# Kernel optimization log

Measured on AMD Instinct MI355X. Metric: run time of the kernel, lower is better.

Reference implementation:

```python
import jax, jax.numpy as jnp
import numpy as np

IN_DIM = 1024
OUT_DIM = 1024
NUM_COEFFS = 32 + 3  # grid_size + spline_order


def setup_inputs() -> dict:
    key = jax.random.key(0)
    k1, k2, k3 = jax.random.split(key, 3)
    x = jax.random.normal(k1, (4096, IN_DIM), dtype=jnp.float32)
    spline_weight = jax.random.normal(k2, (IN_DIM, OUT_DIM, NUM_COEFFS), dtype=jnp.float32) * 0.1
    base_scale = jax.random.normal(k3, (IN_DIM, OUT_DIM), dtype=jnp.float32) * 0.1
    grid = jnp.linspace(-1.0, 1.0, NUM_COEFFS, dtype=jnp.float32)
    return {"x": x, "spline_weight": spline_weight, "base_scale": base_scale, "grid": grid}


def _b_spline_cubic(x, grid):
    # x: [b, i] -> basis [b, i, c]
    h = 2.0 / (NUM_COEFFS - 1)
    dist = jnp.abs(x[..., None] - grid) / h
    inner = 2.0 / 3.0 - dist * dist + dist * dist * dist * 0.5
    t = 2.0 - dist
    outer = t * t * t / 6.0
    return jnp.where(dist < 1.0, inner, jnp.where(dist < 2.0, outer, 0.0))


def reference(x, spline_weight, base_scale, grid):
    x_norm = jnp.clip(x, -0.99, 0.99)
    base_act = jax.nn.silu(x_norm)                      # [b, i]
    base_out = jnp.einsum('bi,ij->bj', base_act, base_scale)
    basis = _b_spline_cubic(x_norm, grid)               # [b, i, c]
    spline_out = jnp.einsum('bic,ijc->bj', basis, spline_weight)
    return base_out + spline_out
```

## Files before the change

### kernel.cpp

```cpp
#include <hip/hip_runtime.h>
#include <hip/hip_bf16.h>


#define IN_DIM 1024
#define OUT_DIM 1024
#define NC 35
#define KPI 36
#define KTOT (IN_DIM * KPI)
#define NW (KTOT / 32)
#define MROWS 4096
#define BM 256
#define BN 256
#define BK 32
#define NSPLIT 4
#define WPC (NW / NSPLIT)

typedef __attribute__((ext_vector_type(8))) __bf16 bf16x8;
typedef __attribute__((ext_vector_type(4))) float f32x4;

__device__ __forceinline__ unsigned short f2bf(float f) {
  unsigned int u = __builtin_bit_cast(unsigned int, f);
  u = (u + 0x7FFFu + ((u >> 16) & 1u)) >> 16;
  return (unsigned short)u;
}

__device__ __forceinline__ uint4 pack8(const unsigned short* v) {
  uint4 t4;
  t4.x = (unsigned)v[0] | ((unsigned)v[1] << 16);
  t4.y = (unsigned)v[2] | ((unsigned)v[3] << 16);
  t4.z = (unsigned)v[4] | ((unsigned)v[5] << 16);
  t4.w = (unsigned)v[6] | ((unsigned)v[7] << 16);
  return t4;
}

__global__ __launch_bounds__(256) void prep_w2(const float* __restrict__ sw,
                                               const float* __restrict__ bs,
                                               unsigned short* __restrict__ w2) {
  const int tid = threadIdx.x;
  const int w = blockIdx.x;
  const int n = blockIdx.y * 256 + tid;
  const int k0 = w * 32;
  const int i0 = k0 / KPI;
  const int off0 = k0 - i0 * KPI;
  const int split = (KPI - off0 < 32) ? (KPI - off0) : 32;
  const int i1 = (i0 + 1 < IN_DIM) ? (i0 + 1) : i0;
  const float* p0 = sw + ((size_t)i0 * OUT_DIM + n) * NC;
  const float* p1 = sw + ((size_t)i1 * OUT_DIM + n) * NC;
  const float bsv = bs[(size_t)i0 * OUT_DIM + n];
  const int swz = (tid >> 1) & 3;

  unsigned short v[32];
#pragma unroll
  for (int kk = 0; kk < 32; ++kk) {
    const int c = off0 + kk;
    const bool ph0 = (kk < split);
    const float* base = ph0 ? p0 : p1;
    const int idx = ph0 ? (c < NC ? c : 0) : (kk - split);
    float fv = base[idx];
    if (ph0 && c == NC) fv = bsv;
    v[kk] = f2bf(fv);
  }
  uint4* dst = (uint4*)(w2 + ((size_t)w * OUT_DIM + n) * 32);
#pragma unroll
  for (int j = 0; j < 4; ++j) dst[j ^ swz] = pack8(&v[8 * j]);
}

__global__ __launch_bounds__(256) void prep_a2t(const float* __restrict__ x,
                                                unsigned short* __restrict__ a2) {
  const int tid = threadIdx.x;
  const int g = blockIdx.x;
  const int b = blockIdx.y * 256 + tid;
  const int i0 = g * 8;
  const int w0 = g * 9;
  const int swz = (tid >> 1) & 3;

  float4 xa = *(const float4*)(x + (size_t)b * IN_DIM + i0);
  float4 xb = *(const float4*)(x + (size_t)b * IN_DIM + i0 + 4);
  const float xv[8] = {xa.x, xa.y, xa.z, xa.w, xb.x, xb.y, xb.z, xb.w};

  int si[8];
  unsigned short tb0[8], tb1[8], tb2[8], tb3[8], sgb[8];
#pragma unroll
  for (int q = 0; q < 8; ++q) {
    float xn = fminf(fmaxf(xv[q], -0.99f), 0.99f);
    float u = (xn + 1.0f) * 17.0f;
    float sf = floorf(u);
    si[q] = (int)sf;
    float f = u - sf, gg = 1.0f - f;
    float f2 = f * f, g2 = gg * gg;
    tb0[q] = f2bf(g2 * gg * (1.f / 6.f));
    tb1[q] = f2bf(0.66666667f - f2 + 0.5f * f2 * f);
    tb2[q] = f2bf(0.66666667f - g2 + 0.5f * g2 * gg);
    tb3[q] = f2bf(f2 * f * (1.f / 6.f));
    sgb[q] = f2bf(xn / (1.0f + __expf(-xn)));
  }

#pragma unroll
  for (int wl = 0; wl < 9; ++wl) {
    unsigned short v[32];
#pragma unroll
    for (int kk = 0; kk < 32; ++kk) {
      const int kr = wl * 32 + kk;
      const int q = kr / KPI;
      const int c = kr % KPI;
      unsigned short val;
      if (c == NC) {
        val = sgb[q];
      } else {
        int rel = c - (si[q] - 1);
        val = (rel == 0) ? tb0[q]
            : (rel == 1) ? tb1[q]
            : (rel == 2) ? tb2[q]
            : (rel == 3) ? tb3[q] : (unsigned short)0;
      }
      v[kk] = val;
    }
    uint4* dst = (uint4*)(a2 + ((size_t)(w0 + wl) * MROWS + b) * 32);
#pragma unroll
    for (int j = 0; j < 4; ++j) dst[j ^ swz] = pack8(&v[8 * j]);
  }
}

__global__ __launch_bounds__(512) void kan_gemm5(const unsigned short* __restrict__ A2,
                                                 const unsigned short* __restrict__ W2,
                                                 float* __restrict__ out) {
  __shared__ __align__(16) unsigned short As[3][BM * BK];
  __shared__ __align__(16) unsigned short Ws[3][BN * BK];

  const int tid = threadIdx.x;
  const int mt = blockIdx.x, nt = blockIdx.y, kc = blockIdx.z;

  const int lane = tid & 63;
  const int wid = tid >> 6;
  const int wm = (wid & 3) * 64;
  const int wn = (wid >> 2) * 128;
  const int lm = lane & 15;
  const int quad = lane >> 4;
  const int koS = (quad ^ ((lm >> 1) & 3)) * 8;

  f32x4 acc[4][8];
#pragma unroll
  for (int a = 0; a < 4; ++a)
#pragma unroll
    for (int b = 0; b < 8; ++b) acc[a][b] = f32x4{0.f, 0.f, 0.f, 0.f};

  const unsigned short* Abase = A2 + (size_t)(mt * BM) * 32 + lane * 8;
  const unsigned short* Wbase = W2 + (size_t)(nt * BN) * 32 + lane * 8;

  auto issue = [&](int buf, int w) {
    const size_t aoff = (size_t)w * (MROWS * 32);
    const size_t woff = (size_t)w * (OUT_DIM * 32);
#pragma unroll
    for (int c = 0; c < 2; ++c) {
      const int g = wid * 2 + c;
      __builtin_amdgcn_global_load_lds(
          (const __attribute__((address_space(1))) unsigned int*)(Abase + aoff + (size_t)g * 512),
          (__attribute__((address_space(3))) unsigned int*)(&As[buf][g * 512]),
          16, 0, 0);
      __builtin_amdgcn_global_load_lds(
          (const __attribute__((address_space(1))) unsigned int*)(Wbase + woff + (size_t)g * 512),
          (__attribute__((address_space(3))) unsigned int*)(&Ws[buf][g * 512]),
          16, 0, 0);
    }
  };

  issue(0, kc * WPC);
  int cur = 0, nxt = 1;
  for (int step = 0; step < WPC; ++step) {
    if (step + 1 < WPC) {
      issue(nxt, kc * WPC + step + 1);
      asm volatile("s_waitcnt vmcnt(4) lgkmcnt(0)\ns_barrier" ::: "memory");
    } else {
      asm volatile("s_waitcnt vmcnt(0) lgkmcnt(0)\ns_barrier" ::: "memory");
    }

    uint4 af[4];
#pragma unroll
    for (int mi = 0; mi < 4; ++mi)
      af[mi] = *(const uint4*)(&As[cur][(wm + mi * 16 + lm) * BK + koS]);
#pragma unroll
    for (int h = 0; h < 2; ++h) {
      uint4 bfr[4];
#pragma unroll
      for (int nj = 0; nj < 4; ++nj)
        bfr[nj] = *(const uint4*)(&Ws[cur][(wn + h * 64 + nj * 16 + lm) * BK + koS]);
#pragma unroll
      for (int mi = 0; mi < 4; ++mi)
#pragma unroll
        for (int nj = 0; nj < 4; ++nj)
          acc[mi][h * 4 + nj] = __builtin_amdgcn_mfma_f32_16x16x32_bf16(
              __builtin_bit_cast(bf16x8, af[mi]), __builtin_bit_cast(bf16x8, bfr[nj]),
              acc[mi][h * 4 + nj], 0, 0, 0);
    }

    cur = nxt;
    nxt = (nxt == 2) ? 0 : nxt + 1;
  }

#pragma unroll
  for (int mi = 0; mi < 4; ++mi)
#pragma unroll
    for (int ni = 0; ni < 8; ++ni)
#pragma unroll
      for (int r = 0; r < 4; ++r) {
        int row = mt * BM + wm + mi * 16 + quad * 4 + r;
        int col = nt * BN + wn + ni * 16 + lm;
        atomicAdd(&out[(size_t)row * OUT_DIM + col], acc[mi][ni][r]);
      }
}

#define FB_BM 128
#define FB_BN 128
#define FB_BKPA 40
#define FB_KCH 9216
#define FB_NSTEP 288

__global__ __launch_bounds__(256) void prep_wb_fb(const float* __restrict__ sw,
                                                  const float* __restrict__ bs,
                                                  unsigned short* __restrict__ wb) {
  int id = blockIdx.x * 256 + threadIdx.x;
  int i = id & (IN_DIM - 1);
  int n = id >> 10;
  const float* s = sw + (size_t)i * (OUT_DIM * NC) + (size_t)n * NC;
  unsigned short v[KPI];
#pragma unroll
  for (int c = 0; c < NC; ++c) v[c] = f2bf(s[c]);
  v[NC] = f2bf(bs[(size_t)i * OUT_DIM + n]);
  uint2* dst = (uint2*)(wb + (size_t)n * KTOT + (size_t)i * KPI);
#pragma unroll
  for (int w = 0; w < 9; ++w) {
    uint2 t;
    t.x = (unsigned)v[4 * w + 0] | ((unsigned)v[4 * w + 1] << 16);
    t.y = (unsigned)v[4 * w + 2] | ((unsigned)v[4 * w + 3] << 16);
    dst[w] = t;
  }
}

template <bool USE_WB>
__global__ __launch_bounds__(256) void kan_gemm_fb(const float* __restrict__ x,
                                                   const unsigned short* __restrict__ wb,
                                                   const float* __restrict__ sw,
                                                   const float* __restrict__ bs,
                                                   float* __restrict__ out) {
  __shared__ __align__(16) unsigned short As[FB_BM * FB_BKPA];
  __shared__ __align__(16) unsigned short Wsm[FB_BN * FB_BKPA];

  const int tid = threadIdx.x;
  const int mt = blockIdx.x, nt = blockIdx.y, kc = blockIdx.z;
  const int sb = tid & 127;
  const int shalf = tid >> 7;
  const int klo = shalf * 16;
  const int wrow = tid >> 1;
  const int whal = tid & 1;
  const int lane = tid & 63;
  const int wid = tid >> 6;
  const int wm = (wid & 1) * 64;
  const int wn = (wid >> 1) * 64;
  const int lm = lane & 15;
  const int quad = lane >> 4;
  const int ko = quad * 8;

  f32x4 acc[4][4];
#pragma unroll
  for (int a = 0; a < 4; ++a)
#pragma unroll
    for (int b = 0; b < 4; ++b) acc[a][b] = f32x4{0.f, 0.f, 0.f, 0.f};

  const float* xrow = x + (size_t)(mt * FB_BM + sb) * IN_DIM;

  for (int step = 0; step < FB_NSTEP; ++step) {
    const int kbase = kc * FB_KCH + step * BK;
    {
      uint4 z = make_uint4(0, 0, 0, 0);
      uint4* az = (uint4*)(&As[sb * FB_BKPA + klo]);
      az[0] = z;
      az[1] = z;
    }
    {
      const int ilo = kbase / KPI;
      const int ihi = (kbase + BK - 1) / KPI;
      for (int ii = ilo; ii <= ihi; ++ii) {
        float xv = xrow[ii];
        float xn = fminf(fmaxf(xv, -0.99f), 0.99f);
        float u = (xn + 1.0f) * 17.0f;
        float sf = floorf(u);
        int s = (int)sf;
        float f = u - sf, g = 1.0f - f;
        float f2 = f * f, g2 = g * g;
        float v0 = g2 * g * (1.f / 6.f);
        float v1 = 0.66666667f - f2 + 0.5f * f2 * f;
        float v2 = 0.66666667f - g2 + 0.5f * g2 * g;
        float v3 = f2 * f * (1.f / 6.f);
        float sig = xn / (1.0f + __expf(-xn));
        const int kb0 = ii * KPI - kbase;
#pragma unroll
        for (int t = 0; t < 4; ++t) {
          int c = s - 1 + t;
          float v = (t == 0) ? v0 : (t == 1) ? v1 : (t == 2) ? v2 : v3;
          int kq = kb0 + c;
          if (c >= 0 && c < NC && kq >= klo && kq < klo + 16)
            As[sb * FB_BKPA + kq] = f2bf(v);
        }
        int kqb = kb0 + NC;
        if (kqb >= klo && kqb < klo + 16) As[sb * FB_BKPA + kqb] = f2bf(sig);
      }
    }
    if (USE_WB) {
      const unsigned short* src = wb + (size_t)(nt * FB_BN + wrow) * KTOT + kbase + whal * 16;
      uint4 w0 = ((const uint4*)src)[0];
      uint4 w1 = ((const uint4*)src)[1];
      uint4* wd = (uint4*)(&Wsm[wrow * FB_BKPA + whal * 16]);
      wd[0] = w0;
      wd[1] = w1;
    } else {
      const int j = nt * FB_BN + wrow;
      unsigned int p[8];
#pragma unroll
      for (int q = 0; q < 8; ++q) {
        unsigned int lohi = 0;
#pragma unroll
        for (int h = 0; h < 2; ++h) {
          int k = kbase + whal * 16 + q * 2 + h;
          int i = k / KPI;
          int c = k - i * KPI;
          float v = (c < NC) ? sw[(size_t)i * (OUT_DIM * NC) + (size_t)j * NC + c]
                             : bs[(size_t)i * OUT_DIM + j];
          lohi |= ((unsigned int)f2bf(v)) << (16 * h);
        }
        p[q] = lohi;
      }
      uint4* wd = (uint4*)(&Wsm[wrow * FB_BKPA + whal * 16]);
      wd[0] = make_uint4(p[0], p[1], p[2], p[3]);
      wd[1] = make_uint4(p[4], p[5], p[6], p[7]);
    }

    __syncthreads();

    uint4 af[4], bfr[4];
#pragma unroll
    for (int mi = 0; mi < 4; ++mi)
      af[mi] = *(const uint4*)(&As[(wm + mi * 16 + lm) * FB_BKPA + ko]);
#pragma unroll
    for (int ni = 0; ni < 4; ++ni)
      bfr[ni] = *(const uint4*)(&Wsm[(wn + ni * 16 + lm) * FB_BKPA + ko]);
#pragma unroll
    for (int mi = 0; mi < 4; ++mi)
#pragma unroll
      for (int ni = 0; ni < 4; ++ni)
        acc[mi][ni] = __builtin_amdgcn_mfma_f32_16x16x32_bf16(
            __builtin_bit_cast(bf16x8, af[mi]), __builtin_bit_cast(bf16x8, bfr[ni]),
            acc[mi][ni], 0, 0, 0);

    __syncthreads();
  }

#pragma unroll
  for (int mi = 0; mi < 4; ++mi)
#pragma unroll
    for (int ni = 0; ni < 4; ++ni)
#pragma unroll
      for (int r = 0; r < 4; ++r) {
        int row = mt * FB_BM + wm + mi * 16 + quad * 4 + r;
        int col = nt * FB_BN + wn + ni * 16 + lm;
        atomicAdd(&out[(size_t)row * OUT_DIM + col], acc[mi][ni][r]);
      }
}

extern "C" void kernel_launch(void* const* d_in, const int* in_sizes, int n_in,
                              void* d_out, int out_size, void* d_ws, size_t ws_size,
                              hipStream_t stream) {
  const float* x = (const float*)d_in[0];
  const float* sw = (const float*)d_in[1];
  const float* bs = (const float*)d_in[2];
  float* out = (float*)d_out;

  hipMemsetAsync(d_out, 0, (size_t)MROWS * OUT_DIM * sizeof(float), stream);

  const size_t WB_BYTES = (size_t)NW * OUT_DIM * 32 * sizeof(unsigned short);
  const size_t A_BYTES = (size_t)NW * MROWS * 32 * sizeof(unsigned short);

  if (ws_size >= WB_BYTES + A_BYTES) {
    unsigned short* w2 = (unsigned short*)d_ws;
    unsigned short* a2 = (unsigned short*)((char*)d_ws + WB_BYTES);
    prep_w2<<<dim3(NW, OUT_DIM / 256), 256, 0, stream>>>(sw, bs, w2);
    prep_a2t<<<dim3(KTOT / 288, MROWS / 256), 256, 0, stream>>>(x, a2);
    kan_gemm5<<<dim3(MROWS / BM, OUT_DIM / BN, NSPLIT), 512, 0, stream>>>(a2, w2, out);
  } else if (ws_size >= WB_BYTES) {
    unsigned short* wbp = (unsigned short*)d_ws;
    prep_wb_fb<<<(IN_DIM * OUT_DIM) / 256, 256, 0, stream>>>(sw, bs, wbp);
    kan_gemm_fb<true><<<dim3(32, 8, 4), 256, 0, stream>>>(x, wbp, sw, bs, out);
  } else {
    kan_gemm_fb<false><<<dim3(32, 8, 4), 256, 0, stream>>>(x, nullptr, sw, bs, out);
  }
}
```

Measured before the change: 707.8 us.

## Fuse B-spline basis construction into GEMM, drop materialized A operand

Removes the separate prep kernel that wrote the expanded bf16 basis matrix (about 300MB) and instead computes basis values per row inside the GEMM main loop. Each thread builds packed bf16 tables for two consecutive inputs and assembles its 32-wide K slice directly into shared memory, overlapping this with the async weight loads. This saves a large global write and read of the A operand, at the cost of extra ALU work and register pressure inside the MFMA loop, plus per-step waitcnt tuning. The intermediate fallback path is also removed.

```diff
diff --git a/kernel.cpp b/kernel.cpp
--- a/kernel.cpp
+++ b/kernel.cpp
@@ -65,63 +65,40 @@
   for (int j = 0; j < 4; ++j) dst[j ^ swz] = pack8(&v[8 * j]);
 }
 
-__global__ __launch_bounds__(256) void prep_a2t(const float* __restrict__ x,
-                                                unsigned short* __restrict__ a2) {
-  const int tid = threadIdx.x;
-  const int g = blockIdx.x;
-  const int b = blockIdx.y * 256 + tid;
-  const int i0 = g * 8;
-  const int w0 = g * 9;
-  const int swz = (tid >> 1) & 3;
-
-  float4 xa = *(const float4*)(x + (size_t)b * IN_DIM + i0);
-  float4 xb = *(const float4*)(x + (size_t)b * IN_DIM + i0 + 4);
-  const float xv[8] = {xa.x, xa.y, xa.z, xa.w, xb.x, xb.y, xb.z, xb.w};
-
-  int si[8];
-  unsigned short tb0[8], tb1[8], tb2[8], tb3[8], sgb[8];
-#pragma unroll
-  for (int q = 0; q < 8; ++q) {
-    float xn = fminf(fmaxf(xv[q], -0.99f), 0.99f);
-    float u = (xn + 1.0f) * 17.0f;
-    float sf = floorf(u);
-    si[q] = (int)sf;
-    float f = u - sf, gg = 1.0f - f;
-    float f2 = f * f, g2 = gg * gg;
-    tb0[q] = f2bf(g2 * gg * (1.f / 6.f));
-    tb1[q] = f2bf(0.66666667f - f2 + 0.5f * f2 * f);
-    tb2[q] = f2bf(0.66666667f - g2 + 0.5f * g2 * gg);
-    tb3[q] = f2bf(f2 * f * (1.f / 6.f));
-    sgb[q] = f2bf(xn / (1.0f + __expf(-xn)));
-  }
-
-#pragma unroll
-  for (int wl = 0; wl < 9; ++wl) {
-    unsigned short v[32];
-#pragma unroll
-    for (int kk = 0; kk < 32; ++kk) {
-      const int kr = wl * 32 + kk;
-      const int q = kr / KPI;
-      const int c = kr % KPI;
-      unsigned short val;
-      if (c == NC) {
-        val = sgb[q];
-      } else {
-        int rel = c - (si[q] - 1);
-        val = (rel == 0) ? tb0[q]
-            : (rel == 1) ? tb1[q]
-            : (rel == 2) ? tb2[q]
-            : (rel == 3) ? tb3[q] : (unsigned short)0;
-      }
-      v[kk] = val;
-    }
-    uint4* dst = (uint4*)(a2 + ((size_t)(w0 + wl) * MROWS + b) * 32);
-#pragma unroll
-    for (int j = 0; j < 4; ++j) dst[j ^ swz] = pack8(&v[8 * j]);
-  }
-}
-
-__global__ __launch_bounds__(512) void kan_gemm5(const unsigned short* __restrict__ A2,
+struct Tab {
+  unsigned Dm1, D0, D1, D2, D3;
+  unsigned SG;
+  int si;
+};
+
+__device__ __forceinline__ Tab mktab(float xv) {
+  float xn = fminf(fmaxf(xv, -0.99f), 0.99f);
+  float u = (xn + 1.0f) * 17.0f;
+  float sf = floorf(u);
+  int si = (int)sf;
+  float f = u - sf, g = 1.0f - f;
+  float f2 = f * f, g2 = g * g;
+  float t0 = g2 * g * (1.f / 6.f);
+  float t1 = 0.66666667f - f2 + 0.5f * f2 * f;
+  float t2 = 0.66666667f - g2 + 0.5f * g2 * g;
+  float t3 = f2 * f * (1.f / 6.f);
+  if (si == 0) t0 = 0.f;
+  if (si == 33) t3 = 0.f;
+  float sg = xn / (1.0f + __expf(-xn));
+  unsigned P01 = (unsigned)f2bf(t0) | ((unsigned)f2bf(t1) << 16);
+  unsigned P23 = (unsigned)f2bf(t2) | ((unsigned)f2bf(t3) << 16);
+  Tab t;
+  t.Dm1 = P01 << 16;
+  t.D0 = P01;
+  t.D1 = (P01 >> 16) | (P23 << 16);
+  t.D2 = P23;
+  t.D3 = P23 >> 16;
+  t.SG = (unsigned)f2bf(sg);
+  t.si = si;
+  return t;
+}
+
+__global__ __launch_bounds__(512) void kan_gemm6(const float* __restrict__ x,
                                                  const unsigned short* __restrict__ W2,
                                                  float* __restrict__ out) {
   __shared__ __align__(16) unsigned short As[3][BM * BK];
@@ -138,25 +115,26 @@
   const int quad = lane >> 4;
   const int koS = (quad ^ ((lm >> 1) & 3)) * 8;
 
+  const int r = tid & 255;
+  const int h = tid >> 8;
+  const int hbase = h * 16;
+  const int swzA = (r >> 1) & 3;
+  const int posA = (2 * h) ^ swzA;
+  const int posB = (2 * h + 1) ^ swzA;
+  const float* xrow = x + (size_t)(mt * BM + r) * IN_DIM;
+
   f32x4 acc[4][8];
 #pragma unroll
   for (int a = 0; a < 4; ++a)
 #pragma unroll
     for (int b = 0; b < 8; ++b) acc[a][b] = f32x4{0.f, 0.f, 0.f, 0.f};
 
-  const unsigned short* Abase = A2 + (size_t)(mt * BM) * 32 + lane * 8;
   const unsigned short* Wbase = W2 + (size_t)(nt * BN) * 32 + lane * 8;
-
-  auto issue = [&](int buf, int w) {
-    const size_t aoff = (size_t)w * (MROWS * 32);
+  auto issueW = [&](int buf, int w) {
     const size_t woff = (size_t)w * (OUT_DIM * 32);
 #pragma unroll
     for (int c = 0; c < 2; ++c) {
       const int g = wid * 2 + c;
-      __builtin_amdgcn_global_load_lds(
-          (const __attribute__((address_space(1))) unsigned int*)(Abase + aoff + (size_t)g * 512),
-          (__attribute__((address_space(3))) unsigned int*)(&As[buf][g * 512]),
-          16, 0, 0);
       __builtin_amdgcn_global_load_lds(
           (const __attribute__((address_space(1))) unsigned int*)(Wbase + woff + (size_t)g * 512),
           (__attribute__((address_space(3))) unsigned int*)(&Ws[buf][g * 512]),
@@ -164,12 +142,66 @@
     }
   };
 
-  issue(0, kc * WPC);
+  int i0 = (kc * WPC * 32) / KPI;
+  int c0 = kc * WPC * 32 - i0 * KPI;
+
+  float xc = xrow[i0];
+  float xd = xrow[(i0 + 1 < IN_DIM) ? i0 + 1 : IN_DIM - 1];
+  float xN = xrow[(i0 + 2 < IN_DIM) ? i0 + 2 : IN_DIM - 1];
+  Tab T0 = mktab(xc);
+  Tab T1 = mktab(xd);
+
+  auto assembleA = [&](int buf) {
+    const int J0 = hbase + c0 + 1 - T0.si;
+    const int J1 = hbase + c0 - 35 - T1.si;
+    const int sl = 35 - c0 - hbase;
+    unsigned pr[8];
+#pragma unroll
+    for (int p = 0; p < 8; ++p) {
+      const int tl0 = J0 + 2 * p;
+      const int tl1 = J1 + 2 * p;
+      unsigned v = (tl0 == -1) ? T0.Dm1
+                 : (tl0 == 0)  ? T0.D0
+                 : (tl0 == 1)  ? T0.D1
+                 : (tl0 == 2)  ? T0.D2
+                 : (tl0 == 3)  ? T0.D3
+                 : (tl1 == -1) ? T1.Dm1
+                 : (tl1 == 0)  ? T1.D0
+                 : (tl1 == 1)  ? T1.D1
+                 : (tl1 == 2)  ? T1.D2
+                 : (tl1 == 3)  ? T1.D3
+                 : 0u;
+      if (sl == 2 * p)     v = (v & 0xFFFF0000u) | T0.SG;
+      if (sl == 2 * p + 1) v = (v & 0x0000FFFFu) | (T0.SG << 16);
+      pr[p] = v;
+    }
+    *(uint4*)(&As[buf][r * BK + posA * 8]) = make_uint4(pr[0], pr[1], pr[2], pr[3]);
+    *(uint4*)(&As[buf][r * BK + posB * 8]) = make_uint4(pr[4], pr[5], pr[6], pr[7]);
+  };
+
+  assembleA(0);
+  issueW(0, kc * WPC);
+
   int cur = 0, nxt = 1;
   for (int step = 0; step < WPC; ++step) {
     if (step + 1 < WPC) {
-      issue(nxt, kc * WPC + step + 1);
-      asm volatile("s_waitcnt vmcnt(4) lgkmcnt(0)\ns_barrier" ::: "memory");
+      int c0n = c0 + 32;
+      const bool rot = (c0n >= KPI);
+      if (rot) {
+        c0 = c0n - KPI;
+        ++i0;
+        T0 = T1;
+        T1 = mktab(xN);
+        xN = xrow[(i0 + 2 < IN_DIM) ? i0 + 2 : IN_DIM - 1];
+      } else {
+        c0 = c0n;
+      }
+      issueW(nxt, kc * WPC + step + 1);
+      assembleA(nxt);
+      if (rot)
+        asm volatile("s_waitcnt vmcnt(3) lgkmcnt(0)\ns_barrier" ::: "memory");
+      else
+        asm volatile("s_waitcnt vmcnt(2) lgkmcnt(0)\ns_barrier" ::: "memory");
     } else {
       asm volatile("s_waitcnt vmcnt(0) lgkmcnt(0)\ns_barrier" ::: "memory");
     }
@@ -179,18 +211,18 @@
     for (int mi = 0; mi < 4; ++mi)
       af[mi] = *(const uint4*)(&As[cur][(wm + mi * 16 + lm) * BK + koS]);
 #pragma unroll
-    for (int h = 0; h < 2; ++h) {
+    for (int hh = 0; hh < 2; ++hh) {
       uint4 bfr[4];
 #pragma unroll
       for (int nj = 0; nj < 4; ++nj)
-        bfr[nj] = *(const uint4*)(&Ws[cur][(wn + h * 64 + nj * 16 + lm) * BK + koS]);
+        bfr[nj] = *(const uint4*)(&Ws[cur][(wn + hh * 64 + nj * 16 + lm) * BK + koS]);
 #pragma unroll
       for (int mi = 0; mi < 4; ++mi)
 #pragma unroll
         for (int nj = 0; nj < 4; ++nj)
-          acc[mi][h * 4 + nj] = __builtin_amdgcn_mfma_f32_16x16x32_bf16(
+          acc[mi][hh * 4 + nj] = __builtin_amdgcn_mfma_f32_16x16x32_bf16(
               __builtin_bit_cast(bf16x8, af[mi]), __builtin_bit_cast(bf16x8, bfr[nj]),
-              acc[mi][h * 4 + nj], 0, 0, 0);
+              acc[mi][hh * 4 + nj], 0, 0, 0);
     }
 
     cur = nxt;
@@ -202,10 +234,10 @@
 #pragma unroll
     for (int ni = 0; ni < 8; ++ni)
 #pragma unroll
-      for (int r = 0; r < 4; ++r) {
-        int row = mt * BM + wm + mi * 16 + quad * 4 + r;
+      for (int rr = 0; rr < 4; ++rr) {
+        int row = mt * BM + wm + mi * 16 + quad * 4 + rr;
         int col = nt * BN + wn + ni * 16 + lm;
-        atomicAdd(&out[(size_t)row * OUT_DIM + col], acc[mi][ni][r]);
+        atomicAdd(&out[(size_t)row * OUT_DIM + col], acc[mi][ni][rr]);
       }
 }
 
@@ -214,27 +246,6 @@
 #define FB_BKPA 40
 #define FB_KCH 9216
 #define FB_NSTEP 288
-
-__global__ __launch_bounds__(256) void prep_wb_fb(const float* __restrict__ sw,
-                                                  const float* __restrict__ bs,
-                                                  unsigned short* __restrict__ wb) {
-  int id = blockIdx.x * 256 + threadIdx.x;
-  int i = id & (IN_DIM - 1);
-  int n = id >> 10;
-  const float* s = sw + (size_t)i * (OUT_DIM * NC) + (size_t)n * NC;
-  unsigned short v[KPI];
-#pragma unroll
-  for (int c = 0; c < NC; ++c) v[c] = f2bf(s[c]);
-  v[NC] = f2bf(bs[(size_t)i * OUT_DIM + n]);
-  uint2* dst = (uint2*)(wb + (size_t)n * KTOT + (size_t)i * KPI);
-#pragma unroll
-  for (int w = 0; w < 9; ++w) {
-    uint2 t;
-    t.x = (unsigned)v[4 * w + 0] | ((unsigned)v[4 * w + 1] << 16);
-    t.y = (unsigned)v[4 * w + 2] | ((unsigned)v[4 * w + 3] << 16);
-    dst[w] = t;
-  }
-}
 
 template <bool USE_WB>
 __global__ __launch_bounds__(256) void kan_gemm_fb(const float* __restrict__ x,
@@ -305,27 +316,20 @@
         if (kqb >= klo && kqb < klo + 16) As[sb * FB_BKPA + kqb] = f2bf(sig);
       }
     }
-    if (USE_WB) {
-      const unsigned short* src = wb + (size_t)(nt * FB_BN + wrow) * KTOT + kbase + whal * 16;
-      uint4 w0 = ((const uint4*)src)[0];
-      uint4 w1 = ((const uint4*)src)[1];
-      uint4* wd = (uint4*)(&Wsm[wrow * FB_BKPA + whal * 16]);
-      wd[0] = w0;
-      wd[1] = w1;
-    } else {
+    {
       const int j = nt * FB_BN + wrow;
       unsigned int p[8];
 #pragma unroll
       for (int q = 0; q < 8; ++q) {
         unsigned int lohi = 0;
 #pragma unroll
-        for (int h = 0; h < 2; ++h) {
-          int k = kbase + whal * 16 + q * 2 + h;
+        for (int hh = 0; hh < 2; ++hh) {
+          int k = kbase + whal * 16 + q * 2 + hh;
           int i = k / KPI;
           int c = k - i * KPI;
           float v = (c < NC) ? sw[(size_t)i * (OUT_DIM * NC) + (size_t)j * NC + c]
                              : bs[(size_t)i * OUT_DIM + j];
-          lohi |= ((unsigned int)f2bf(v)) << (16 * h);
+          lohi |= ((unsigned int)f2bf(v)) << (16 * hh);
         }
         p[q] = lohi;
       }
@@ -359,10 +363,10 @@
 #pragma unroll
     for (int ni = 0; ni < 4; ++ni)
 #pragma unroll
-      for (int r = 0; r < 4; ++r) {
-        int row = mt * FB_BM + wm + mi * 16 + quad * 4 + r;
+      for (int rr = 0; rr < 4; ++rr) {
+        int row = mt * FB_BM + wm + mi * 16 + quad * 4 + rr;
         int col = nt * FB_BN + wn + ni * 16 + lm;
-        atomicAdd(&out[(size_t)row * OUT_DIM + col], acc[mi][ni][r]);
+        atomicAdd(&out[(size_t)row * OUT_DIM + col], acc[mi][ni][rr]);
       }
 }
 
@@ -377,18 +381,11 @@
   hipMemsetAsync(d_out, 0, (size_t)MROWS * OUT_DIM * sizeof(float), stream);
 
   const size_t WB_BYTES = (size_t)NW * OUT_DIM * 32 * sizeof(unsigned short);
-  const size_t A_BYTES = (size_t)NW * MROWS * 32 * sizeof(unsigned short);
-
-  if (ws_size >= WB_BYTES + A_BYTES) {
+
+  if (ws_size >= WB_BYTES) {
     unsigned short* w2 = (unsigned short*)d_ws;
-    unsigned short* a2 = (unsigned short*)((char*)d_ws + WB_BYTES);
     prep_w2<<<dim3(NW, OUT_DIM / 256), 256, 0, stream>>>(sw, bs, w2);
-    prep_a2t<<<dim3(KTOT / 288, MROWS / 256), 256, 0, stream>>>(x, a2);
-    kan_gemm5<<<dim3(MROWS / BM, OUT_DIM / BN, NSPLIT), 512, 0, stream>>>(a2, w2, out);
-  } else if (ws_size >= WB_BYTES) {
-    unsigned short* wbp = (unsigned short*)d_ws;
-    prep_wb_fb<<<(IN_DIM * OUT_DIM) / 256, 256, 0, stream>>>(sw, bs, wbp);
-    kan_gemm_fb<true><<<dim3(32, 8, 4), 256, 0, stream>>>(x, wbp, sw, bs, out);
+    kan_gemm6<<<dim3(MROWS / BM, OUT_DIM / BN, NSPLIT), 512, 0, stream>>>(x, w2, out);
   } else {
     kan_gemm_fb<false><<<dim3(32, 8, 4), 256, 0, stream>>>(x, nullptr, sw, bs, out);
   }
```

New measurement: 1.225 ms. 1.73x slower.
